# Performance work log

Hardware: AMD Instinct MI355X
Metric: run time of the kernel (lower is better)

## Reference

```python
import jax, jax.numpy as jnp
import numpy as np

B, N, D, HEAD = 16, 1024, 512, 256  # hidden_size=512, gcn_layer=2 -> head_dim=256


def _xavier(key, shape):
    lim = (6.0 / (shape[0] + shape[-1])) ** 0.5
    return jax.random.uniform(key, shape, jnp.float32, -lim, lim)


def setup_inputs() -> dict:
    key = jax.random.key(0)
    ks = jax.random.split(key, 10)
    fi_lim = (6.0 / (D + 1)) ** 0.5
    return {
        "x": jax.random.normal(ks[0], (B, N, D), jnp.float32),
        "tp_w": _xavier(ks[1], (D, D)), "tp_b": jnp.zeros((D,), jnp.float32),
        "tc_w": _xavier(ks[2], (D, D)), "tc_b": jnp.zeros((D,), jnp.float32),
        "fi_w": jax.random.uniform(ks[3], (D,), jnp.float32, -fi_lim, fi_lim),
        "bil_w": _xavier(ks[4], (D, D)),
        "gcn_w0": _xavier(ks[5], (D, HEAD)), "gcn_b0": jnp.zeros((HEAD,), jnp.float32),
        "gcn_w1": _xavier(ks[6], (D + HEAD, HEAD)), "gcn_b1": jnp.zeros((HEAD,), jnp.float32),
        "out_w": _xavier(ks[7], (D, D)), "out_b": jnp.zeros((D,), jnp.float32),
    }


def reference(x, tp_w, tp_b, tc_w, tc_b, fi_w, bil_w,
              gcn_w0, gcn_b0, gcn_w1, gcn_b1, out_w, out_b):
    Bb, Nn, Dd = x.shape
    # ---- StructInduction: matrix-tree latent structure ----
    tp = jnp.tanh(x @ tp_w + tp_b)                      # [B,N,D]
    tc = jnp.tanh(x @ tc_w + tc_b)                      # [B,N,D]
    # original expands BOTH tp and tc along dim 2 -> f_ij[b,i,j] = s[b,i]
    s = jnp.einsum('bnd,de,bne->bn', tp, bil_w, tc)     # [B,N]
    f_i = jnp.exp(x @ fi_w)                             # [B,N] root scores
    eye = jnp.eye(Nn, dtype=x.dtype)
    A = jnp.exp(s)[:, :, None] * (1.0 - eye)            # [B,N,N], zero diagonal
    col_sum = A.sum(axis=1)                             # [B,N] sum over dim 1
    L = -A + col_sum[:, None, :] * eye                  # Laplacian
    L = L.at[:, 0, :].set(f_i)                          # replace row 0 with root scores
    Linv = jnp.linalg.inv(L)                            # [B,N,N]
    d0 = f_i * Linv[:, :, 0]                            # [B,N]
    diag = jnp.diagonal(Linv, axis1=-2, axis2=-1)       # [B,N]
    tmp1 = A * diag[:, None, :]                         # A[b,i,j]*Linv_diag[b,j]
    tmp2 = A * jnp.swapaxes(Linv, 1, 2)                 # A[b,i,j]*Linv[b,j,i]
    mask1 = jnp.concatenate([jnp.zeros((Nn, 1), x.dtype),
                             jnp.ones((Nn, Nn - 1), x.dtype)], axis=1)  # zero col 0
    mask2 = mask1.T                                     # zero row 0
    dx = mask1 * tmp1 - mask2 * tmp2                    # [B,N,N]
    d = jnp.concatenate([d0[:, None, :], dx], axis=1)   # [B,N+1,N]
    df = jnp.swapaxes(d, 1, 2)                          # [B,N,N+1]
    adj = df[:, :, 1:]                                  # [B,N,N] latent adjacency
    # ---- GraphConvLayer (self_loop=True, dropout = identity / eval) ----
    denom = adj.sum(axis=2, keepdims=True) + 1.0        # [B,N,1]
    outputs = x
    cache = [x]
    outs = []
    for (W, b) in ((gcn_w0, gcn_b0), (gcn_w1, gcn_b1)):
        Ax = adj @ outputs                              # [B,N,in_dim]
        AxW = (Ax @ W + b) + (outputs @ W + b)          # neighbor + self loop
        g = jax.nn.relu(AxW / denom)                    # [B,N,HEAD]
        cache.append(g)
        outputs = jnp.concatenate(cache, axis=2)        # densely connected
        outs.append(g)
    gcn_out = jnp.concatenate(outs, axis=2) + x         # [B,N,D] residual
    return gcn_out @ out_w + out_b
```

## Files before the change

kernel.cpp:

```cpp
#include <hip/hip_runtime.h>
#include <cmath>

#define BN   16384
#define DD   512
#define HEADN 256

typedef unsigned short ushort;
typedef short short8 __attribute__((ext_vector_type(8)));
typedef float floatx4 __attribute__((ext_vector_type(4)));
typedef unsigned short ushort4v __attribute__((ext_vector_type(4)));
typedef unsigned short ushort8v __attribute__((ext_vector_type(8)));

__device__ __forceinline__ ushort f2bf(float v) {
    unsigned int u = __float_as_uint(v);
    unsigned int r = u + 0x7FFFu + ((u >> 16) & 1u);
    return (ushort)(r >> 16);
}
__device__ __forceinline__ float bf2f(ushort u) {
    return __uint_as_float(((unsigned int)u) << 16);
}
__device__ __forceinline__ float tanh_fast(float x) {
    float xc = fminf(fmaxf(x, -15.0f), 15.0f);
    float e = __expf(2.0f * xc);
    return (e - 1.0f) * __builtin_amdgcn_rcpf(e + 1.0f);
}

template <int TM, int TN, int KK, int EPI>
__global__ __launch_bounds__(256) void gemm_lds(
    const ushort* __restrict__ A, int lda,
    const ushort* __restrict__ Bt, int N,
    const float* __restrict__ bias,
    const float* __restrict__ denom,
    const ushort* __restrict__ tcb, int tcld,
    float* __restrict__ s_arr,
    void* __restrict__ Cout, int ldc,
    const ushort* __restrict__ xgb, int xoff, ushort* __restrict__ gout)
{
    constexpr int MI = TM / 32;
    constexpr int NI = TN / 32;
    constexpr int ROWS = TM + TN;
    constexpr int CPT = (ROWS * 8) / 256;
    constexpr int MT = 16384 / TM;
    constexpr int MT_PER_BAND = MT / 8;
    constexpr int NK = KK >> 6;
    __shared__ ushort S[2 * ROWS * 64];

    const int g = blockIdx.x;
    const int band = g & 7, within = g >> 3;
    const int nt = within / MT_PER_BAND;
    const int mt = band * MT_PER_BAND + (within - nt * MT_PER_BAND);
    const int m0 = mt * TM, n0 = nt * TN;
    const int w = threadIdx.x >> 6, L = threadIdx.x & 63;
    const int wr0 = (w >> 1) * (TM / 2), wc0 = (w & 1) * (TN / 2);
    const int lrow = L & 15, quad = L >> 4;

    const ushort* gbase[CPT];
#pragma unroll
    for (int rr = 0; rr < CPT; ++rr) {
        const int chunk = rr * 256 + (w << 6) + L;
        const int row = chunk >> 3, slot = chunk & 7;
        const int ca = slot ^ ((row >> 1) & 7);
        gbase[rr] = (row < TM)
            ? A  + (size_t)(m0 + row) * lda    + (ca << 3)
            : Bt + (size_t)(n0 + row - TM) * KK + (ca << 3);
    }

    floatx4 zero4 = {0.0f, 0.0f, 0.0f, 0.0f};
    floatx4 acc[MI][NI];
#pragma unroll
    for (int i = 0; i < MI; ++i)
#pragma unroll
        for (int j = 0; j < NI; ++j) acc[i][j] = zero4;

    auto stage = [&](int buf, int k0) {
        ushort* Sd = S + buf * (ROWS * 64);
#pragma unroll
        for (int rr = 0; rr < CPT; ++rr) {
            __builtin_amdgcn_global_load_lds(
                (const __attribute__((address_space(1))) unsigned int*)(gbase[rr] + k0),
                (__attribute__((address_space(3))) unsigned int*)(Sd + (rr * 256 + (w << 6)) * 8),
                16, 0, 0);
        }
    };

    stage(0, 0);
#pragma unroll
    for (int kk = 0; kk < NK; ++kk) {
        __syncthreads();
        if (kk + 1 < NK) stage((kk + 1) & 1, (kk + 1) << 6);

        const ushort* Sc = S + (kk & 1) * (ROWS * 64);
        short8 af[2][MI], bfr[2][NI];
#pragma unroll
        for (int ks = 0; ks < 2; ++ks) {
#pragma unroll
            for (int mi = 0; mi < MI; ++mi) {
                const int row = wr0 + (mi << 4) + lrow;
                const int slot = ((ks << 2) + quad) ^ ((row >> 1) & 7);
                af[ks][mi] = *(const short8*)(Sc + row * 64 + (slot << 3));
            }
#pragma unroll
            for (int ni = 0; ni < NI; ++ni) {
                const int row = TM + wc0 + (ni << 4) + lrow;
                const int slot = ((ks << 2) + quad) ^ ((row >> 1) & 7);
                bfr[ks][ni] = *(const short8*)(Sc + row * 64 + (slot << 3));
            }
        }
#pragma unroll
        for (int ks = 0; ks < 2; ++ks)
#pragma unroll
            for (int mi = 0; mi < MI; ++mi)
#pragma unroll
                for (int ni = 0; ni < NI; ++ni)
                    acc[mi][ni] = __builtin_amdgcn_mfma_f32_16x16x32_bf16(
                        af[ks][mi], bfr[ks][ni], acc[mi][ni], 0, 0, 0);
    }

    if constexpr (EPI == 3) {
#pragma unroll
        for (int mi = 0; mi < MI; ++mi) {
            float rs[4] = {0.f, 0.f, 0.f, 0.f};
#pragma unroll
            for (int ni = 0; ni < NI; ++ni) {
                const int gc = n0 + wc0 + (ni << 4) + lrow;
#pragma unroll
                for (int p = 0; p < 4; ++p) {
                    const int gr = m0 + wr0 + (mi << 4) + (quad << 2) + p;
                    rs[p] += acc[mi][ni][p] * bf2f(tcb[(size_t)gr * tcld + gc]);
                }
            }
#pragma unroll
            for (int p = 0; p < 4; ++p)
#pragma unroll
                for (int o = 1; o < 16; o <<= 1) rs[p] += __shfl_xor(rs[p], o);
            if (lrow == 0) {
#pragma unroll
                for (int p = 0; p < 4; ++p)
                    atomicAdd(s_arr + m0 + wr0 + (mi << 4) + (quad << 2) + p, rs[p]);
            }
        }
    } else {
#pragma unroll
        for (int mi = 0; mi < MI; ++mi) {
#pragma unroll
            for (int p = 0; p < 4; ++p) {
                const int gr = m0 + wr0 + (mi << 4) + (quad << 2) + p;
                const float rdv = (EPI == 2) ? __builtin_amdgcn_rcpf(denom[gr]) : 1.0f;
#pragma unroll
                for (int ni = 0; ni < NI; ++ni) {
                    const int gc = n0 + wc0 + (ni << 4) + lrow;
                    const float v = acc[mi][ni][p];
                    if constexpr (EPI == 0) {
                        ((float*)Cout)[(size_t)gr * ldc + gc] = v + bias[gc];
                    } else if constexpr (EPI == 1) {
                        ((ushort*)Cout)[(size_t)gr * ldc + gc] = f2bf(tanh_fast(v + bias[gc]));
                    } else {
                        float u = (v + 2.0f * bias[gc]) * rdv;
                        u = u > 0.0f ? u : 0.0f;
                        if (Cout)
                            ((ushort*)Cout)[(size_t)gr * ldc + gc] = f2bf(u);
                        if (gout)
                            gout[(size_t)gr * 512 + xoff + gc] =
                                f2bf(u + bf2f(xgb[(size_t)gr * 512 + xoff + gc]));
                    }
                }
            }
        }
    }
}

__global__ __launch_bounds__(256) void prep_k(
    const float* __restrict__ x, const float* __restrict__ fiw,
    ushort* __restrict__ xb, float* __restrict__ fdot,
    const float* __restrict__ tp_w, const float* __restrict__ tc_w,
    const float* __restrict__ bilw, const float* __restrict__ ow,
    const float* __restrict__ w0, const float* __restrict__ w1,
    const float* __restrict__ tp_b, const float* __restrict__ tc_b,
    ushort* __restrict__ tptcwT, ushort* __restrict__ bilwT,
    ushort* __restrict__ owT, ushort* __restrict__ w0T,
    ushort* __restrict__ w1T, float* __restrict__ bias2,
    float* __restrict__ zstats, int zcount)
{
    const int blk0 = blockIdx.x;
    if (blk0 < 4096) {
        const int wv = threadIdx.x >> 6, L = threadIdx.x & 63;
        const int r = (blk0 << 2) + wv;
        const float* xr = x + (size_t)r * DD;
        const int c0 = L << 3;
        float4 v0 = *(const float4*)(xr + c0);
        float4 v1 = *(const float4*)(xr + c0 + 4);
        float4 f0 = *(const float4*)(fiw + c0);
        float4 f1 = *(const float4*)(fiw + c0 + 4);
        float d = v0.x * f0.x + v0.y * f0.y + v0.z * f0.z + v0.w * f0.w
                + v1.x * f1.x + v1.y * f1.y + v1.z * f1.z + v1.w * f1.w;
        ushort8v o;
        o[0] = f2bf(v0.x); o[1] = f2bf(v0.y); o[2] = f2bf(v0.z); o[3] = f2bf(v0.w);
        o[4] = f2bf(v1.x); o[5] = f2bf(v1.y); o[6] = f2bf(v1.z); o[7] = f2bf(v1.w);
        *(ushort8v*)(xb + (size_t)r * DD + c0) = o;
#pragma unroll
        for (int off = 32; off > 0; off >>= 1) d += __shfl_xor(d, off);
        if (L == 0) fdot[r] = d;
        return;
    }
    if (blk0 >= 5441) {
        for (int i = (blk0 - 5441) * 256 + threadIdx.x; i < zcount; i += 16 * 256)
            zstats[i] = 0.0f;
        return;
    }
    const int blk = blk0 - 4096;
    if (blk >= 1344) {
        for (int i = threadIdx.x; i < 512; i += 256) {
            bias2[i] = tp_b[i];
            bias2[512 + i] = tc_b[i];
        }
        return;
    }
    const float* W; ushort* Wt; int K, N, local;
    if (blk < 256)       { W = tp_w; Wt = tptcwT;              K = 512; N = 512; local = blk; }
    else if (blk < 512)  { W = tc_w; Wt = tptcwT + 512 * 512;  K = 512; N = 512; local = blk - 256; }
    else if (blk < 768)  { W = bilw; Wt = bilwT;               K = 512; N = 512; local = blk - 512; }
    else if (blk < 1024) { W = ow;   Wt = owT;                 K = 512; N = 512; local = blk - 768; }
    else if (blk < 1152) { W = w0;   Wt = w0T;                 K = 512; N = 256; local = blk - 1024; }
    else                 { W = w1;   Wt = w1T;                 K = 768; N = 256; local = blk - 1152; }

    __shared__ float t[32][33];
    const int nb = N >> 5;
    const int kb = local / nb, nbb = local % nb;
    const int k0 = kb << 5, n0 = nbb << 5;
    const int c = threadIdx.x & 31, r = threadIdx.x >> 5;
#pragma unroll
    for (int i = 0; i < 4; ++i)
        t[r + 8 * i][c] = W[(size_t)(k0 + r + 8 * i) * N + n0 + c];
    __syncthreads();
#pragma unroll
    for (int i = 0; i < 4; ++i)
        Wt[(size_t)(n0 + r + 8 * i) * K + k0 + c] = f2bf(t[c][r + 8 * i]);
}

__global__ __launch_bounds__(1024) void finalize_k(
    const float* __restrict__ s_arr, const float* __restrict__ fdot,
    float* __restrict__ a, float* __restrict__ f,
    float* __restrict__ Sb, float* __restrict__ Hb, float* __restrict__ den)
{
    __shared__ float redS[16], redH[16];
    __shared__ float Hsh;
    const int b = blockIdx.x, t = threadIdx.x;
    const int r = (b << 10) + t;
    const float av = __expf(s_arr[r]), fv = __expf(fdot[r]);
    a[r] = av; f[r] = fv;
    float s1 = av, s2 = av * fv;
#pragma unroll
    for (int o = 32; o > 0; o >>= 1) { s1 += __shfl_xor(s1, o); s2 += __shfl_xor(s2, o); }
    if ((t & 63) == 0) { redS[t >> 6] = s1; redH[t >> 6] = s2; }
    __syncthreads();
    if (t == 0) {
        float S = 0.f, H = 0.f;
        for (int i = 0; i < 16; ++i) { S += redS[i]; H += redH[i]; }
        Sb[b] = S; Hb[b] = H; Hsh = H;
    }
    __syncthreads();
    den[r] = 2.0f - av * fv * __builtin_amdgcn_rcpf(Hsh);
}

__global__ __launch_bounds__(256) void batch_pq(
    const ushort* __restrict__ V, const float* __restrict__ a, const float* __restrict__ f,
    float* __restrict__ P, float* __restrict__ Q, int C)
{
    __shared__ float redP[256][4];
    __shared__ float redQ[256][4];
    const int b = blockIdx.x >> 4;
    const int chunk = blockIdx.x & 15;
    const int c4cnt = C >> 2;
    const int rg = 256 / c4cnt;
    const int c4 = threadIdx.x & (c4cnt - 1);
    const int sub = threadIdx.x / c4cnt;
    const ushort* Vb = V + (size_t)b * 1024 * C;
    const float* ab = a + (b << 10);
    const float* fb = f + (b << 10);
    const int n0 = chunk << 6;
    float4 p = {0, 0, 0, 0}, q = {0, 0, 0, 0};
    for (int n = n0 + sub; n < n0 + 64; n += rg) {
        const float av = ab[n], afv = av * fb[n];
        ushort4v u = *(const ushort4v*)(Vb + (size_t)n * C + (c4 << 2));
        float4 v = {bf2f(u[0]), bf2f(u[1]), bf2f(u[2]), bf2f(u[3])};
        p.x += av * v.x; p.y += av * v.y; p.z += av * v.z; p.w += av * v.w;
        q.x += afv * v.x; q.y += afv * v.y; q.z += afv * v.z; q.w += afv * v.w;
    }
    redP[threadIdx.x][0] = p.x; redP[threadIdx.x][1] = p.y;
    redP[threadIdx.x][2] = p.z; redP[threadIdx.x][3] = p.w;
    redQ[threadIdx.x][0] = q.x; redQ[threadIdx.x][1] = q.y;
    redQ[threadIdx.x][2] = q.z; redQ[threadIdx.x][3] = q.w;
    __syncthreads();
    if (sub == 0) {
        for (int s = 1; s < rg; ++s) {
            const int t2 = threadIdx.x + s * c4cnt;
            p.x += redP[t2][0]; p.y += redP[t2][1]; p.z += redP[t2][2]; p.w += redP[t2][3];
            q.x += redQ[t2][0]; q.y += redQ[t2][1]; q.z += redQ[t2][2]; q.w += redQ[t2][3];
        }
        float* Pp = P + b * C + (c4 << 2);
        float* Qp = Q + b * C + (c4 << 2);
        atomicAdd(Pp + 0, p.x); atomicAdd(Pp + 1, p.y);
        atomicAdd(Pp + 2, p.z); atomicAdd(Pp + 3, p.w);
        atomicAdd(Qp + 0, q.x); atomicAdd(Qp + 1, q.y);
        atomicAdd(Qp + 2, q.z); atomicAdd(Qp + 3, q.w);
    }
}

__global__ __launch_bounds__(256) void mix_k(
    const ushort* __restrict__ V, const float* __restrict__ P, const float* __restrict__ Q,
    const float* __restrict__ a, const float* __restrict__ f,
    const float* __restrict__ Sb, const float* __restrict__ Hb,
    ushort* __restrict__ outb, int C, int ldo, int co)
{
    const int idx = blockIdx.x * 256 + threadIdx.x;
    const int c4c = C >> 2;
    const int r = idx / c4c, c4 = idx - r * c4c;
    const int b = r >> 10;
    const float av = a[r], fv = f[r], S = Sb[b], H = Hb[b];
    const float rS = __builtin_amdgcn_rcpf(S);
    const float beta = av * rS * __builtin_amdgcn_rcpf(H);
    const float alpha = 1.0f - av * rS;
    const float cp = rS - beta * fv;
    ushort4v u = *(const ushort4v*)(V + (size_t)r * C + (c4 << 2));
    float4 v = {bf2f(u[0]), bf2f(u[1]), bf2f(u[2]), bf2f(u[3])};
    const float* Pp = P + b * C + (c4 << 2);
    const float* Qp = Q + b * C + (c4 << 2);
    ushort4v o;
    o[0] = f2bf(alpha * v.x + cp * Pp[0] + beta * Qp[0]);
    o[1] = f2bf(alpha * v.y + cp * Pp[1] + beta * Qp[1]);
    o[2] = f2bf(alpha * v.z + cp * Pp[2] + beta * Qp[2]);
    o[3] = f2bf(alpha * v.w + cp * Pp[3] + beta * Qp[3]);
    *(ushort4v*)(outb + (size_t)r * ldo + co + (c4 << 2)) = o;
}

extern "C" void kernel_launch(void* const* d_in, const int* in_sizes, int n_in,
                              void* d_out, int out_size, void* d_ws, size_t ws_size,
                              hipStream_t stream)
{
    (void)in_sizes; (void)n_in; (void)out_size; (void)ws_size;
    const float* x    = (const float*)d_in[0];
    const float* tp_w = (const float*)d_in[1];
    const float* tp_b = (const float*)d_in[2];
    const float* tc_w = (const float*)d_in[3];
    const float* tc_b = (const float*)d_in[4];
    const float* fi_w = (const float*)d_in[5];
    const float* bilw = (const float*)d_in[6];
    const float* w0   = (const float*)d_in[7];
    const float* b0   = (const float*)d_in[8];
    const float* w1   = (const float*)d_in[9];
    const float* b1   = (const float*)d_in[10];
    const float* ow   = (const float*)d_in[11];
    const float* ob   = (const float*)d_in[12];

    char* W = (char*)d_ws;
    ushort* xb    = (ushort*)W;
    ushort* gcnb  = xb;
    ushort* tptcb = (ushort*)(W + ((size_t)16 << 20));
    ushort* Hbuf  = tptcb;
    ushort* g0b   = (ushort*)(W + ((size_t)48 << 20));
    ushort* tptcwT= (ushort*)(W + ((size_t)56 << 20));
    ushort* bilwT = tptcwT + 524288;
    ushort* owT   = bilwT + 262144;
    ushort* w0T   = owT + 262144;
    ushort* w1T   = w0T + 131072;
    float*  bias2 = (float*)(w1T + 196608);
    float* stats  = (float*)(W + ((size_t)60 << 20));
    float* s_arr  = stats;
    float* P0     = s_arr + 16384;
    float* Q0     = P0 + 8192;
    float* P1     = Q0 + 8192;
    float* Q1     = P1 + 4096;
    const int zcount = 16384 + 2 * 8192 + 2 * 4096;
    float* fdot   = Q1 + 4096;
    float* arr_a  = fdot + BN;
    float* arr_f  = arr_a + BN;
    float* arr_den= arr_f + BN;
    float* Sb     = arr_den + BN;
    float* Hb     = Sb + 16;

    prep_k<<<5457, 256, 0, stream>>>(x, fi_w, xb, fdot, tp_w, tc_w, bilw, ow, w0, w1,
                                     tp_b, tc_b, tptcwT, bilwT, owT, w0T, w1T, bias2,
                                     s_arr, zcount);
    gemm_lds<64, 64, 512, 1><<<4096, 256, 0, stream>>>(xb, 512, tptcwT, 1024, bias2,
        nullptr, nullptr, 0, nullptr, tptcb, 1024, nullptr, 0, nullptr);
    gemm_lds<64, 64, 512, 3><<<2048, 256, 0, stream>>>(tptcb, 1024, bilwT, 512, nullptr,
        nullptr, tptcb + 512, 1024, s_arr, nullptr, 0, nullptr, 0, nullptr);
    finalize_k<<<16, 1024, 0, stream>>>(s_arr, fdot, arr_a, arr_f, Sb, Hb, arr_den);
    batch_pq<<<256, 256, 0, stream>>>(xb, arr_a, arr_f, P0, Q0, 512);
    mix_k<<<8192, 256, 0, stream>>>(xb, P0, Q0, arr_a, arr_f, Sb, Hb, Hbuf, 512, 768, 0);
    gemm_lds<64, 64, 512, 2><<<1024, 256, 0, stream>>>(Hbuf, 768, w0T, 256, b0,
        arr_den, nullptr, 0, nullptr, g0b, 256, xb, 0, gcnb);
    batch_pq<<<256, 256, 0, stream>>>(g0b, arr_a, arr_f, P1, Q1, 256);
    mix_k<<<4096, 256, 0, stream>>>(g0b, P1, Q1, arr_a, arr_f, Sb, Hb, Hbuf, 256, 768, 512);
    gemm_lds<64, 64, 768, 2><<<1024, 256, 0, stream>>>(Hbuf, 768, w1T, 256, b1,
        arr_den, nullptr, 0, nullptr, nullptr, 0, xb, 256, gcnb);
    gemm_lds<64, 64, 512, 0><<<2048, 256, 0, stream>>>(gcnb, 512, owT, 512, ob,
        nullptr, nullptr, 0, nullptr, (float*)d_out, 512, nullptr, 0, nullptr);
}
```

Baseline: 234.7 us.

## Fuse layer-1 P/Q reduction into GCN layer-0 GEMM epilogue via atomics

The layer-0 GCN GEMM gets a new epilogue variant that accumulates the a- and a*f-weighted column sums of its ReLU output and atomically adds them into P1/Q1. This removes the separate batch_pq launch that re-read g0b. It also splits the remaining layer-0 batch_pq over twice as many blocks (32 chunks per batch) for more parallelism. In exchange it adds atomics and register pressure to the GEMM epilogue, and the sums now come from fp32 values rather than the bf16-rounded g0b, which slightly changes numerics.

Result: no change. 234.8 us (+0.1%).

```diff
diff --git a/kernel.cpp b/kernel.cpp
--- a/kernel.cpp
+++ b/kernel.cpp
@@ -34,7 +34,9 @@
     const ushort* __restrict__ tcb, int tcld,
     float* __restrict__ s_arr,
     void* __restrict__ Cout, int ldc,
-    const ushort* __restrict__ xgb, int xoff, ushort* __restrict__ gout)
+    const ushort* __restrict__ xgb, int xoff, ushort* __restrict__ gout,
+    const float* __restrict__ a_arr, const float* __restrict__ f_arr,
+    float* __restrict__ Pq, float* __restrict__ Qq)
 {
     constexpr int MI = TM / 32;
     constexpr int NI = TN / 32;
@@ -140,12 +142,21 @@
             }
         }
     } else {
+        float sp[NI], sq[NI];
+#pragma unroll
+        for (int ni = 0; ni < NI; ++ni) { sp[ni] = 0.0f; sq[ni] = 0.0f; }
 #pragma unroll
         for (int mi = 0; mi < MI; ++mi) {
 #pragma unroll
             for (int p = 0; p < 4; ++p) {
                 const int gr = m0 + wr0 + (mi << 4) + (quad << 2) + p;
-                const float rdv = (EPI == 2) ? __builtin_amdgcn_rcpf(denom[gr]) : 1.0f;
+                const float rdv = (EPI == 2 || EPI == 4)
+                                  ? __builtin_amdgcn_rcpf(denom[gr]) : 1.0f;
+                float av = 0.0f, afv = 0.0f;
+                if constexpr (EPI == 4) {
+                    av = a_arr[gr];
+                    afv = av * f_arr[gr];
+                }
 #pragma unroll
                 for (int ni = 0; ni < NI; ++ni) {
                     const int gc = n0 + wc0 + (ni << 4) + lrow;
@@ -157,12 +168,32 @@
                     } else {
                         float u = (v + 2.0f * bias[gc]) * rdv;
                         u = u > 0.0f ? u : 0.0f;
+                        if constexpr (EPI == 4) {
+                            sp[ni] += av * u;
+                            sq[ni] += afv * u;
+                        }
                         if (Cout)
                             ((ushort*)Cout)[(size_t)gr * ldc + gc] = f2bf(u);
                         if (gout)
                             gout[(size_t)gr * 512 + xoff + gc] =
                                 f2bf(u + bf2f(xgb[(size_t)gr * 512 + xoff + gc]));
                     }
+                }
+            }
+        }
+        if constexpr (EPI == 4) {
+            const int b = m0 >> 10;
+#pragma unroll
+            for (int ni = 0; ni < NI; ++ni) {
+#pragma unroll
+                for (int o = 16; o < 64; o <<= 1) {
+                    sp[ni] += __shfl_xor(sp[ni], o);
+                    sq[ni] += __shfl_xor(sq[ni], o);
+                }
+                if (quad == 0) {
+                    const int gc = n0 + wc0 + (ni << 4) + lrow;
+                    atomicAdd(Pq + b * HEADN + gc, sp[ni]);
+                    atomicAdd(Qq + b * HEADN + gc, sq[ni]);
                 }
             }
         }
@@ -262,14 +293,16 @@
     den[r] = 2.0f - av * fv * __builtin_amdgcn_rcpf(Hsh);
 }
 
+template <int CH>
 __global__ __launch_bounds__(256) void batch_pq(
     const ushort* __restrict__ V, const float* __restrict__ a, const float* __restrict__ f,
     float* __restrict__ P, float* __restrict__ Q, int C)
 {
     __shared__ float redP[256][4];
     __shared__ float redQ[256][4];
-    const int b = blockIdx.x >> 4;
-    const int chunk = blockIdx.x & 15;
+    const int b = blockIdx.x / CH;
+    const int chunk = blockIdx.x - b * CH;
+    constexpr int RPC = 1024 / CH;
     const int c4cnt = C >> 2;
     const int rg = 256 / c4cnt;
     const int c4 = threadIdx.x & (c4cnt - 1);
@@ -277,9 +310,9 @@
     const ushort* Vb = V + (size_t)b * 1024 * C;
     const float* ab = a + (b << 10);
     const float* fb = f + (b << 10);
-    const int n0 = chunk << 6;
+    const int n0 = chunk * RPC;
     float4 p = {0, 0, 0, 0}, q = {0, 0, 0, 0};
-    for (int n = n0 + sub; n < n0 + 64; n += rg) {
+    for (int n = n0 + sub; n < n0 + RPC; n += rg) {
         const float av = ab[n], afv = av * fb[n];
         ushort4v u = *(const ushort4v*)(Vb + (size_t)n * C + (c4 << 2));
         float4 v = {bf2f(u[0]), bf2f(u[1]), bf2f(u[2]), bf2f(u[3])};
@@ -382,18 +415,22 @@
                                      tp_b, tc_b, tptcwT, bilwT, owT, w0T, w1T, bias2,
                                      s_arr, zcount);
     gemm_lds<64, 64, 512, 1><<<4096, 256, 0, stream>>>(xb, 512, tptcwT, 1024, bias2,
-        nullptr, nullptr, 0, nullptr, tptcb, 1024, nullptr, 0, nullptr);
+        nullptr, nullptr, 0, nullptr, tptcb, 1024, nullptr, 0, nullptr,
+        nullptr, nullptr, nullptr, nullptr);
     gemm_lds<64, 64, 512, 3><<<2048, 256, 0, stream>>>(tptcb, 1024, bilwT, 512, nullptr,
-        nullptr, tptcb + 512, 1024, s_arr, nullptr, 0, nullptr, 0, nullptr);
+        nullptr, tptcb + 512, 1024, s_arr, nullptr, 0, nullptr, 0, nullptr,
+        nullptr, nullptr, nullptr, nullptr);
     finalize_k<<<16, 1024, 0, stream>>>(s_arr, fdot, arr_a, arr_f, Sb, Hb, arr_den);
-    batch_pq<<<256, 256, 0, stream>>>(xb, arr_a, arr_f, P0, Q0, 512);
+    batch_pq<32><<<512, 256, 0, stream>>>(xb, arr_a, arr_f, P0, Q0, 512);
     mix_k<<<8192, 256, 0, stream>>>(xb, P0, Q0, arr_a, arr_f, Sb, Hb, Hbuf, 512, 768, 0);
-    gemm_lds<64, 64, 512, 2><<<1024, 256, 0, stream>>>(Hbuf, 768, w0T, 256, b0,
-        arr_den, nullptr, 0, nullptr, g0b, 256, xb, 0, gcnb);
-    batch_pq<<<256, 256, 0, stream>>>(g0b, arr_a, arr_f, P1, Q1, 256);
+    gemm_lds<64, 64, 512, 4><<<1024, 256, 0, stream>>>(Hbuf, 768, w0T, 256, b0,
+        arr_den, nullptr, 0, nullptr, g0b, 256, xb, 0, gcnb,
+        arr_a, arr_f, P1, Q1);
     mix_k<<<4096, 256, 0, stream>>>(g0b, P1, Q1, arr_a, arr_f, Sb, Hb, Hbuf, 256, 768, 512);
     gemm_lds<64, 64, 768, 2><<<1024, 256, 0, stream>>>(Hbuf, 768, w1T, 256, b1,
-        arr_den, nullptr, 0, nullptr, nullptr, 0, xb, 256, gcnb);
+        arr_den, nullptr, 0, nullptr, nullptr, 0, xb, 256, gcnb,
+        nullptr, nullptr, nullptr, nullptr);
     gemm_lds<64, 64, 512, 0><<<2048, 256, 0, stream>>>(gcnb, 512, owT, 512, ob,
-        nullptr, nullptr, 0, nullptr, (float*)d_out, 512, nullptr, 0, nullptr);
-}
+        nullptr, nullptr, 0, nullptr, (float*)d_out, 512, nullptr, 0, nullptr,
+        nullptr, nullptr, nullptr, nullptr);
+}
```
